# Kernel tuning notes

Measured on AMD Instinct MI355X. Metric: run time of the kernel, lower is better.

## Reference

```python
import jax, jax.numpy as jnp
import numpy as np

H = 128
V = 50000
B = 128
T_C = 50
T_I = 32
T_Q = 32
EPISODES = 3


def gru_cell(x, h, Wih, Whh, bih, bhh):
    # torch GRUCell math
    gi = x @ Wih.T + bih
    gh = h @ Whh.T + bhh
    ir, iz, inn = jnp.split(gi, 3, axis=-1)
    hr, hz, hn = jnp.split(gh, 3, axis=-1)
    r = jax.nn.sigmoid(ir + hr)
    z = jax.nn.sigmoid(iz + hz)
    n = jnp.tanh(inn + r * hn)
    return (1.0 - z) * n + z * h


def gru_outputs(x, Wih, Whh, bih, bhh):
    # x: (N, T, H) -> hidden at every step, (N, T, H)
    h0 = jnp.zeros((x.shape[0], x.shape[2]), x.dtype)
    def step(h, xt):
        h2 = gru_cell(xt, h, Wih, Whh, bih, bhh)
        return h2, h2
    _, ys = jax.lax.scan(step, h0, jnp.swapaxes(x, 0, 1))
    return jnp.swapaxes(ys, 0, 1)


def setup_inputs():
    key = jax.random.key(0)
    ks = iter(jax.random.split(key, 48))
    s = 0.05
    def mat(shape):
        return (jax.random.normal(next(ks), shape) * s).astype(jnp.float32)
    def gru_p(in_dim):
        return mat((3 * H, in_dim)), mat((3 * H, H)), mat((3 * H,)), mat((3 * H,))
    embed = mat((V, H)).at[0].set(0.0)  # padding_idx=0
    ig_Wih, ig_Whh, ig_bih, ig_bhh = gru_p(H)
    qg_Wih, qg_Whh, qg_bih, qg_bhh = gru_p(H)
    at_Wih, at_Whh, at_bih, at_bhh = gru_p(H)
    me_Wih, me_Whh, me_bih, me_bhh = gru_p(H)
    an_Wih, an_Whh, an_bih, an_bhh = gru_p(2 * H)
    gate_W1 = mat((H, 4 * H)); gate_b1 = mat((H,))
    gate_W2 = mat((1, H)); gate_b2 = mat((1,))
    fc_W = mat((V, H)); fc_b = jnp.zeros((V,), jnp.float32)
    facts = jax.random.randint(next(ks), (B, T_C, T_I), 0, V)
    fact_masks = jnp.zeros((B, T_C, T_I), jnp.int32)  # 0 == real token
    questions = jax.random.randint(next(ks), (B, T_Q), 0, V)
    question_masks = jnp.zeros((B, T_Q), jnp.int32)
    return dict(facts=facts, fact_masks=fact_masks, questions=questions,
                question_masks=question_masks, num_decode=8, embed=embed,
                ig_Wih=ig_Wih, ig_Whh=ig_Whh, ig_bih=ig_bih, ig_bhh=ig_bhh,
                qg_Wih=qg_Wih, qg_Whh=qg_Whh, qg_bih=qg_bih, qg_bhh=qg_bhh,
                at_Wih=at_Wih, at_Whh=at_Whh, at_bih=at_bih, at_bhh=at_bhh,
                me_Wih=me_Wih, me_Whh=me_Whh, me_bih=me_bih, me_bhh=me_bhh,
                an_Wih=an_Wih, an_Whh=an_Whh, an_bih=an_bih, an_bhh=an_bhh,
                gate_W1=gate_W1, gate_b1=gate_b1, gate_W2=gate_W2, gate_b2=gate_b2,
                fc_W=fc_W, fc_b=fc_b)


def reference(facts, fact_masks, questions, question_masks, num_decode, embed,
              ig_Wih, ig_Whh, ig_bih, ig_bhh,
              qg_Wih, qg_Whh, qg_bih, qg_bhh,
              at_Wih, at_Whh, at_bih, at_bhh,
              me_Wih, me_Whh, me_bih, me_bhh,
              an_Wih, an_Whh, an_bih, an_bhh,
              gate_W1, gate_b1, gate_W2, gate_b2, fc_W, fc_b):
    Bv, Tc, Ti = facts.shape
    Hd = embed.shape[1]

    # ---- fact encoding: one batched GRU over all B*T_C facts ----
    f = facts.reshape(Bv * Tc, Ti)
    emb = embed[f]                                            # (B*Tc, Ti, H)
    outs = gru_outputs(emb, ig_Wih, ig_Whh, ig_bih, ig_bhh)
    flen = jnp.sum(fact_masks.reshape(Bv * Tc, Ti) == 0, axis=-1)
    enc_f = jnp.take_along_axis(outs, (flen - 1)[:, None, None], axis=1)[:, 0]
    enc_f = enc_f.reshape(Bv, Tc, Hd)                         # (B, T_C, H)

    # ---- question encoding ----
    qouts = gru_outputs(embed[questions], qg_Wih, qg_Whh, qg_bih, qg_bhh)
    qlen = jnp.sum(question_masks == 0, axis=-1)
    q = jnp.take_along_axis(qouts, (qlen - 1)[:, None, None], axis=1)[:, 0]  # (B, H)

    # ---- episodic memory ----
    memory = q
    facts_t = jnp.swapaxes(enc_f, 0, 1)                       # (T_C, B, H)
    for _ in range(EPISODES):
        m = memory
        def ep_step(h, ft):
            z = jnp.concatenate([ft * q, ft * m, jnp.abs(ft - q), jnp.abs(ft - m)], axis=-1)
            g = jax.nn.sigmoid(jnp.tanh(z @ gate_W1.T + gate_b1) @ gate_W2.T + gate_b2)  # (B,1)
            h2 = gru_cell(ft, h, at_Wih, at_Whh, at_bih, at_bhh)
            return g * h2 + (1.0 - g) * h, None
        e, _ = jax.lax.scan(ep_step, jnp.zeros_like(memory), facts_t)
        memory = gru_cell(e, memory, me_Wih, me_Whh, me_bih, me_bhh)

    # ---- answer decoding (y_{t-1} stays the <s> embedding, as in the source) ----
    y0 = jnp.broadcast_to(embed[2], (Bv, Hd))                 # <s> token id = 2
    yq = jnp.concatenate([y0, q], axis=-1)                    # (B, 2H)
    def dec_step(h, _):
        h2 = gru_cell(yq, h, an_Wih, an_Whh, an_bih, an_bhh)
        return h2, jax.nn.log_softmax(h2 @ fc_W.T + fc_b, axis=-1)
    _, dec = jax.lax.scan(dec_step, memory, None, length=num_decode)  # (T, B, V)
    return jnp.swapaxes(dec, 0, 1).reshape(Bv * num_decode, -1)
```

## Files before the change

kernel.cpp:

```cpp
#include <hip/hip_runtime.h>
#include <math.h>

#define H   128
#define H3  384
#define TC  50
#define TI  32
#define TQ  32
#define NB  128
#define NF  (NB*TC)
#define EPISODES 3
#define LSLICE 25

typedef short  bf16x8 __attribute__((ext_vector_type(8)));
typedef float  f32x4  __attribute__((ext_vector_type(4)));

__device__ __forceinline__ float dot4(float4 a, float4 b) {
  return a.x*b.x + a.y*b.y + a.z*b.z + a.w*b.w;
}
__device__ __forceinline__ float sigm(float x) { return 1.f/(1.f + __expf(-x)); }
__device__ __forceinline__ float tanh_f(float x) { return 1.f - 2.f/(1.f + __expf(2.f*x)); }
__device__ __forceinline__ float gru_comb(float ir, float iz, float inn,
                                          float hr, float hz, float hn, float h) {
  float r = sigm(ir + hr);
  float z = sigm(iz + hz);
  float n = tanh_f(inn + r*hn);
  return (1.f - z)*n + z*h;
}
__device__ __forceinline__ short f2bf(float x) {
  union { float f; unsigned u; } v; v.f = x;
  unsigned r = v.u + 0x7fffu + ((v.u >> 16) & 1u);
  return (short)(r >> 16);
}
__device__ __forceinline__ float bf2f(short s) {
  union { unsigned u; float f; } v; v.u = ((unsigned)(unsigned short)s) << 16;
  return v.f;
}
__device__ __forceinline__ bf16x8 pack8(float4 lo, float4 hi) {
  bf16x8 o;
  o[0]=f2bf(lo.x); o[1]=f2bf(lo.y); o[2]=f2bf(lo.z); o[3]=f2bf(lo.w);
  o[4]=f2bf(hi.x); o[5]=f2bf(hi.y); o[6]=f2bf(hi.z); o[7]=f2bf(hi.w);
  return o;
}

__global__ __launch_bounds__(256) void k_mgemm_bf16(const float* __restrict__ A,
    const float* __restrict__ Bm, const float* __restrict__ bias,
    short* __restrict__ C, int M, int N)
{
  __shared__ __align__(16) short As[64][136];
  __shared__ __align__(16) short Bs[128][136];
  int tid = threadIdx.x;
  int lane = tid & 63, wave = tid >> 6;
  int bm = blockIdx.x, bn = blockIdx.y;
  #pragma unroll
  for (int i = 0; i < 4; ++i) {
    int ch = tid + i*256;
    int r = ch >> 4, e = (ch & 15)*8;
    int gr = bm*64 + r; if (gr > M-1) gr = M-1;
    const float* src = A + (size_t)gr*H + e;
    *(bf16x8*)&As[r][e] = pack8(*(const float4*)src, *(const float4*)(src+4));
  }
  #pragma unroll
  for (int i = 0; i < 8; ++i) {
    int ch = tid + i*256;
    int r = ch >> 4, e = (ch & 15)*8;
    int gn = bn*128 + r; if (gn > N-1) gn = N-1;
    const float* src = Bm + (size_t)gn*H + e;
    *(bf16x8*)&Bs[r][e] = pack8(*(const float4*)src, *(const float4*)(src+4));
  }
  __syncthreads();
  int q = lane >> 4, l15 = lane & 15;
  f32x4 acc[8];
  #pragma unroll
  for (int nt = 0; nt < 8; ++nt) { acc[nt][0]=0.f; acc[nt][1]=0.f; acc[nt][2]=0.f; acc[nt][3]=0.f; }
  int mrow = wave*16 + l15;
  #pragma unroll
  for (int kf = 0; kf < 4; ++kf) {
    bf16x8 a = *(bf16x8*)&As[mrow][q*8 + kf*32];
    #pragma unroll
    for (int nt = 0; nt < 8; ++nt) {
      bf16x8 b = *(bf16x8*)&Bs[nt*16 + l15][q*8 + kf*32];
      acc[nt] = __builtin_amdgcn_mfma_f32_16x16x32_bf16(a, b, acc[nt], 0, 0, 0);
    }
  }
  __syncthreads();
  #pragma unroll
  for (int nt = 0; nt < 8; ++nt) {
    int col = nt*16 + l15;
    float bv = bias[bn*128 + col];
    #pragma unroll
    for (int reg = 0; reg < 4; ++reg)
      Bs[wave*16 + q*4 + reg][col] = f2bf(acc[nt][reg] + bv);
  }
  __syncthreads();
  #pragma unroll
  for (int i = 0; i < 4; ++i) {
    int idx = tid + i*256;
    int r = idx >> 4, e = (idx & 15)*8;
    int gr = bm*64 + r;
    if (gr < M) *(bf16x8*)(C + (size_t)gr*N + bn*128 + e) = *(bf16x8*)&Bs[r][e];
  }
}

__global__ __launch_bounds__(128) void k_gather(const float* __restrict__ embed,
    const int* __restrict__ toks, float* __restrict__ dst)
{
  int b = blockIdx.x;
  int t = toks[b];
  dst[(size_t)b*H + threadIdx.x] = embed[(size_t)t*H + threadIdx.x];
}

__global__ __launch_bounds__(256) void k_copy(const float* __restrict__ src,
    float* __restrict__ dst, int n)
{
  int i = blockIdx.x*256 + threadIdx.x;
  if (i < n) dst[i] = src[i];
}

#define GI_STR 392
__global__ __launch_bounds__(512) void k_recgru2(
    const short* __restrict__ GI, const int* __restrict__ toks,
    const int* __restrict__ masks,
    const float* __restrict__ Whh, const float* __restrict__ bhh,
    float* __restrict__ enc_out, int steps)
{
  __shared__ __align__(16) short hsb[2][16][136];
  __shared__ __align__(16) short gib[2][16][GI_STR];
  __shared__ int ltoks[16*TI];
  __shared__ int enc_step_s[16];
  int tid = threadIdx.x;
  int lane = tid & 63, wave = tid >> 6;
  int q = lane >> 4, l15 = lane & 15;
  int seq0 = blockIdx.x * 16;

  for (int i = tid; i < 2*16*136; i += 512) ((short*)hsb)[i] = 0;
  if (toks) for (int i = tid; i < 16*steps; i += 512)
    ltoks[i] = toks[(size_t)seq0*steps + i];
  if (tid < 16) {
    int fl = 0;
    for (int i = 0; i < steps; ++i) fl += (masks[(size_t)(seq0+tid)*steps + i] == 0);
    int et = fl - 1; if (et < 0) et = 0; if (et >= steps) et = steps-1;
    enc_step_s[tid] = et;
  }
  bf16x8 wfrag[3][4];
  #pragma unroll
  for (int i = 0; i < 3; ++i) {
    int n = 16*wave + 128*i + l15;
    const float* wr = Whh + (size_t)n*H + q*8;
    #pragma unroll
    for (int kf = 0; kf < 4; ++kf)
      wfrag[i][kf] = pack8(*(const float4*)(wr + kf*32), *(const float4*)(wr + kf*32 + 4));
  }
  int c = 16*wave + l15;
  float bh0 = bhh[c], bh1 = bhh[c+H], bh2 = bhh[c+2*H];
  int ch0 = tid, ch1 = tid + 512;
  int r0 = ch0/48, o0 = ch0 - r0*48;
  int r1 = ch1/48, o1 = ch1 - r1*48;
  __syncthreads();
  int es[4];
  #pragma unroll
  for (int reg = 0; reg < 4; ++reg) es[reg] = enc_step_s[q*4 + reg];

  {
    size_t row0 = toks ? (size_t)ltoks[r0*steps] : ((size_t)(seq0 + r0)*steps);
    *(bf16x8*)&gib[0][r0][o0*8] = *((const bf16x8*)(GI + row0*H3) + o0);
    if (tid < 256) {
      size_t row1 = toks ? (size_t)ltoks[r1*steps] : ((size_t)(seq0 + r1)*steps);
      *(bf16x8*)&gib[0][r1][o1*8] = *((const bf16x8*)(GI + row1*H3) + o1);
    }
  }
  __syncthreads();

  float hreg[4] = {0.f, 0.f, 0.f, 0.f};
  for (int t = 0; t < steps; ++t) {
    bf16x8 pf0, pf1;
    bool havepf = (t + 1 < steps);
    if (havepf) {
      size_t row0 = toks ? (size_t)ltoks[r0*steps + t + 1]
                         : ((size_t)(seq0 + r0)*steps + t + 1);
      pf0 = *((const bf16x8*)(GI + row0*H3) + o0);
      if (tid < 256) {
        size_t row1 = toks ? (size_t)ltoks[r1*steps + t + 1]
                           : ((size_t)(seq0 + r1)*steps + t + 1);
        pf1 = *((const bf16x8*)(GI + row1*H3) + o1);
      }
    }
    f32x4 acc[3];
    #pragma unroll
    for (int i = 0; i < 3; ++i) { acc[i][0]=0.f; acc[i][1]=0.f; acc[i][2]=0.f; acc[i][3]=0.f; }
    #pragma unroll
    for (int kf = 0; kf < 4; ++kf) {
      bf16x8 a = *(bf16x8*)&hsb[t & 1][l15][kf*32 + q*8];
      #pragma unroll
      for (int i = 0; i < 3; ++i)
        acc[i] = __builtin_amdgcn_mfma_f32_16x16x32_bf16(a, wfrag[i][kf], acc[i], 0, 0, 0);
    }
    #pragma unroll
    for (int reg = 0; reg < 4; ++reg) {
      int row = q*4 + reg;
      float gr = bf2f(gib[t & 1][row][c]);
      float gz = bf2f(gib[t & 1][row][c + 128]);
      float gn = bf2f(gib[t & 1][row][c + 256]);
      float hnew = gru_comb(gr, gz, gn,
                            acc[0][reg] + bh0, acc[1][reg] + bh1, acc[2][reg] + bh2,
                            hreg[reg]);
      hreg[reg] = hnew;
      hsb[(t + 1) & 1][row][c] = f2bf(hnew);
      if (t == es[reg]) enc_out[(size_t)(seq0 + row)*H + c] = hnew;
    }
    if (havepf) {
      *(bf16x8*)&gib[(t + 1) & 1][r0][o0*8] = pf0;
      if (tid < 256) *(bf16x8*)&gib[(t + 1) & 1][r1][o1*8] = pf1;
    }
    __syncthreads();
  }
}

__global__ __launch_bounds__(128) void k_gatepre(const float* __restrict__ encf,
    const float* __restrict__ qv, const float* __restrict__ W1,
    const float* __restrict__ b1, float* __restrict__ U1)
{
  __shared__ float us[16][H], vs[16][H];
  int tid = threadIdx.x;
  int nt0 = blockIdx.x * 16;
  for (int i = tid; i < 16*H; i += 128) {
    int r = i >> 7, k = i & 127;
    int nt = nt0 + r, n = nt / TC;
    float f = encf[(size_t)nt*H + k];
    float q = qv[(size_t)n*H + k];
    us[r][k] = f*q;
    vs[r][k] = fabsf(f - q);
  }
  __syncthreads();
  int c = tid;
  float acc[16] = {};
  const float* wa = W1 + (size_t)c*(4*H);
  const float* wc = wa + 2*H;
  for (int kk = 0; kk < H; kk += 16) {
    float4 a0 = *(const float4*)(wa + kk);
    float4 a1 = *(const float4*)(wa + kk + 4);
    float4 a2 = *(const float4*)(wa + kk + 8);
    float4 a3 = *(const float4*)(wa + kk + 12);
    float4 c0 = *(const float4*)(wc + kk);
    float4 c1 = *(const float4*)(wc + kk + 4);
    float4 c2 = *(const float4*)(wc + kk + 8);
    float4 c3 = *(const float4*)(wc + kk + 12);
    #pragma unroll
    for (int r = 0; r < 16; ++r) {
      const float* up = &us[r][kk];
      const float* vp = &vs[r][kk];
      acc[r] += dot4(*(const float4*)up,     a0) + dot4(*(const float4*)(up+4), a1)
              + dot4(*(const float4*)(up+8), a2) + dot4(*(const float4*)(up+12),a3)
              + dot4(*(const float4*)vp,     c0) + dot4(*(const float4*)(vp+4), c1)
              + dot4(*(const float4*)(vp+8), c2) + dot4(*(const float4*)(vp+12),c3);
    }
  }
  float bb = b1[c];
  #pragma unroll
  for (int r = 0; r < 16; ++r) U1[(size_t)(nt0 + r)*H + c] = acc[r] + bb;
}

__global__ __launch_bounds__(128) void k_gate(const float* __restrict__ encf,
    const float* __restrict__ mem, const float* __restrict__ W1,
    const float* __restrict__ W2, const float* __restrict__ b2,
    const float* __restrict__ U1, float* __restrict__ gate)
{
  __shared__ float us[16][H], vs[16][H], hid[16][H], parts[16][8];
  int tid = threadIdx.x;
  int nt0 = blockIdx.x * 16;
  for (int i = tid; i < 16*H; i += 128) {
    int r = i >> 7, k = i & 127;
    int nt = nt0 + r, n = nt / TC;
    float f = encf[(size_t)nt*H + k];
    float m = mem[(size_t)n*H + k];
    us[r][k] = f*m;
    vs[r][k] = fabsf(f - m);
  }
  __syncthreads();
  int c = tid;
  float acc[16];
  #pragma unroll
  for (int r = 0; r < 16; ++r) acc[r] = U1[(size_t)(nt0 + r)*H + c];
  const float* wb = W1 + (size_t)c*(4*H) + H;
  const float* wd = W1 + (size_t)c*(4*H) + 3*H;
  for (int kk = 0; kk < H; kk += 16) {
    float4 a0 = *(const float4*)(wb + kk);
    float4 a1 = *(const float4*)(wb + kk + 4);
    float4 a2 = *(const float4*)(wb + kk + 8);
    float4 a3 = *(const float4*)(wb + kk + 12);
    float4 c0 = *(const float4*)(wd + kk);
    float4 c1 = *(const float4*)(wd + kk + 4);
    float4 c2 = *(const float4*)(wd + kk + 8);
    float4 c3 = *(const float4*)(wd + kk + 12);
    #pragma unroll
    for (int r = 0; r < 16; ++r) {
      const float* up = &us[r][kk];
      const float* vp = &vs[r][kk];
      acc[r] += dot4(*(const float4*)up,     a0) + dot4(*(const float4*)(up+4), a1)
              + dot4(*(const float4*)(up+8), a2) + dot4(*(const float4*)(up+12),a3)
              + dot4(*(const float4*)vp,     c0) + dot4(*(const float4*)(vp+4), c1)
              + dot4(*(const float4*)(vp+8), c2) + dot4(*(const float4*)(vp+12),c3);
    }
  }
  #pragma unroll
  for (int r = 0; r < 16; ++r) hid[r][c] = tanh_f(acc[r]);
  __syncthreads();
  {
    int r = tid >> 3, i = tid & 7;
    float p = 0.f;
    for (int k = i*16; k < i*16 + 16; ++k) p += hid[r][k]*W2[k];
    parts[r][i] = p;
  }
  __syncthreads();
  if (tid < 16) {
    float s = b2[0];
    #pragma unroll
    for (int i = 0; i < 8; ++i) s += parts[tid][i];
    gate[nt0 + tid] = sigm(s);
  }
}

__global__ __launch_bounds__(512) void k_episode2(
    const short* __restrict__ GIat, const float* __restrict__ gate,
    const float* __restrict__ at_Whh, const float* __restrict__ at_bhh,
    const float* __restrict__ me_Wih, const float* __restrict__ me_Whh,
    const float* __restrict__ me_bih, const float* __restrict__ me_bhh,
    float* __restrict__ mem)
{
  __shared__ __align__(16) short hsb[2][16][136];
  __shared__ __align__(16) short msb[16][136];
  __shared__ __align__(16) short gib[2][16][GI_STR];
  int tid = threadIdx.x;
  int lane = tid & 63, wave = tid >> 6;
  int q = lane >> 4, l15 = lane & 15;
  int n0 = blockIdx.x * 16;

  for (int i = tid; i < 2*16*136; i += 512) ((short*)hsb)[i] = 0;
  for (int i = tid; i < 16*H; i += 512) {
    int r = i >> 7, cc = i & 127;
    msb[r][cc] = f2bf(mem[(size_t)(n0 + r)*H + cc]);
  }
  bf16x8 wfrag[3][4];
  #pragma unroll
  for (int i = 0; i < 3; ++i) {
    int n = 16*wave + 128*i + l15;
    const float* wr = at_Whh + (size_t)n*H + q*8;
    #pragma unroll
    for (int kf = 0; kf < 4; ++kf)
      wfrag[i][kf] = pack8(*(const float4*)(wr + kf*32), *(const float4*)(wr + kf*32 + 4));
  }
  int c = 16*wave + l15;
  float bh0 = at_bhh[c], bh1 = at_bhh[c+H], bh2 = at_bhh[c+2*H];
  int ch0 = tid, ch1 = tid + 512;
  int r0 = ch0/48, o0 = ch0 - r0*48;
  int r1 = ch1/48, o1 = ch1 - r1*48;
  __syncthreads();

  *(bf16x8*)&gib[0][r0][o0*8] = *((const bf16x8*)(GIat + (size_t)(n0 + r0)*TC*H3) + o0);
  if (tid < 256)
    *(bf16x8*)&gib[0][r1][o1*8] = *((const bf16x8*)(GIat + (size_t)(n0 + r1)*TC*H3) + o1);
  __syncthreads();

  float hreg[4] = {0.f, 0.f, 0.f, 0.f};
  for (int t = 0; t < TC; ++t) {
    bf16x8 pf0, pf1;
    bool havepf = (t + 1 < TC);
    if (havepf) {
      pf0 = *((const bf16x8*)(GIat + ((size_t)(n0 + r0)*TC + t + 1)*H3) + o0);
      if (tid < 256)
        pf1 = *((const bf16x8*)(GIat + ((size_t)(n0 + r1)*TC + t + 1)*H3) + o1);
    }
    f32x4 acc[3];
    #pragma unroll
    for (int i = 0; i < 3; ++i) { acc[i][0]=0.f; acc[i][1]=0.f; acc[i][2]=0.f; acc[i][3]=0.f; }
    #pragma unroll
    for (int kf = 0; kf < 4; ++kf) {
      bf16x8 a = *(bf16x8*)&hsb[t & 1][l15][kf*32 + q*8];
      #pragma unroll
      for (int i = 0; i < 3; ++i)
        acc[i] = __builtin_amdgcn_mfma_f32_16x16x32_bf16(a, wfrag[i][kf], acc[i], 0, 0, 0);
    }
    #pragma unroll
    for (int reg = 0; reg < 4; ++reg) {
      int row = q*4 + reg;
      float g  = gate[(size_t)(n0 + row)*TC + t];
      float gr = bf2f(gib[t & 1][row][c]);
      float gz = bf2f(gib[t & 1][row][c + 128]);
      float gn = bf2f(gib[t & 1][row][c + 256]);
      float h2 = gru_comb(gr, gz, gn,
                          acc[0][reg] + bh0, acc[1][reg] + bh1, acc[2][reg] + bh2,
                          hreg[reg]);
      float hnew = g*h2 + (1.f - g)*hreg[reg];
      hreg[reg] = hnew;
      hsb[(t + 1) & 1][row][c] = f2bf(hnew);
    }
    if (havepf) {
      *(bf16x8*)&gib[(t + 1) & 1][r0][o0*8] = pf0;
      if (tid < 256) *(bf16x8*)&gib[(t + 1) & 1][r1][o1*8] = pf1;
    }
    __syncthreads();
  }
  f32x4 gi_acc[3], gh_acc[3];
  #pragma unroll
  for (int i = 0; i < 3; ++i) {
    gi_acc[i][0]=0.f; gi_acc[i][1]=0.f; gi_acc[i][2]=0.f; gi_acc[i][3]=0.f;
    gh_acc[i][0]=0.f; gh_acc[i][1]=0.f; gh_acc[i][2]=0.f; gh_acc[i][3]=0.f;
  }
  #pragma unroll
  for (int i = 0; i < 3; ++i) {
    int n = 16*wave + 128*i + l15;
    const float* wr = me_Wih + (size_t)n*H + q*8;
    #pragma unroll
    for (int kf = 0; kf < 4; ++kf)
      wfrag[i][kf] = pack8(*(const float4*)(wr + kf*32), *(const float4*)(wr + kf*32 + 4));
  }
  #pragma unroll
  for (int kf = 0; kf < 4; ++kf) {
    bf16x8 a = *(bf16x8*)&hsb[TC & 1][l15][kf*32 + q*8];
    #pragma unroll
    for (int i = 0; i < 3; ++i)
      gi_acc[i] = __builtin_amdgcn_mfma_f32_16x16x32_bf16(a, wfrag[i][kf], gi_acc[i], 0, 0, 0);
  }
  #pragma unroll
  for (int i = 0; i < 3; ++i) {
    int n = 16*wave + 128*i + l15;
    const float* wr = me_Whh + (size_t)n*H + q*8;
    #pragma unroll
    for (int kf = 0; kf < 4; ++kf)
      wfrag[i][kf] = pack8(*(const float4*)(wr + kf*32), *(const float4*)(wr + kf*32 + 4));
  }
  #pragma unroll
  for (int kf = 0; kf < 4; ++kf) {
    bf16x8 a = *(bf16x8*)&msb[l15][kf*32 + q*8];
    #pragma unroll
    for (int i = 0; i < 3; ++i)
      gh_acc[i] = __builtin_amdgcn_mfma_f32_16x16x32_bf16(a, wfrag[i][kf], gh_acc[i], 0, 0, 0);
  }
  float bi0 = me_bih[c], bi1 = me_bih[c+H], bi2 = me_bih[c+2*H];
  float bo0 = me_bhh[c], bo1 = me_bhh[c+H], bo2 = me_bhh[c+2*H];
  #pragma unroll
  for (int reg = 0; reg < 4; ++reg) {
    int row = q*4 + reg;
    float m = mem[(size_t)(n0 + row)*H + c];
    float mnew = gru_comb(gi_acc[0][reg] + bi0, gi_acc[1][reg] + bi1, gi_acc[2][reg] + bi2,
                          gh_acc[0][reg] + bo0, gh_acc[1][reg] + bo1, gh_acc[2][reg] + bo2, m);
    mem[(size_t)(n0 + row)*H + c] = mnew;
  }
}

__global__ __launch_bounds__(384) void k_decode(const float* __restrict__ embed,
    const float* __restrict__ qv, const float* __restrict__ mem,
    const float* __restrict__ an_Wih, const float* __restrict__ an_Whh,
    const float* __restrict__ an_bih, const float* __restrict__ an_bhh,
    float* __restrict__ h2d, int ND)
{
  __shared__ float hs[2][H], qs[2][H], e2[H], ghs[2][H3], gis[2][H3];
  int tid = threadIdx.x;
  int n0 = blockIdx.x * 2;
  if (tid < H) e2[tid] = embed[2*H + tid];
  if (tid < 256) {
    int r = tid >> 7, c = tid & 127;
    hs[r][c] = mem[(size_t)(n0 + r)*H + c];
    qs[r][c] = qv[(size_t)(n0 + r)*H + c];
  }
  __syncthreads();
  {
    const float* wp = an_Wih + (size_t)tid*(2*H);
    float se = 0.f, sq0 = 0.f, sq1 = 0.f;
    for (int kk = 0; kk < H; kk += 16) {
      float4 w0 = *(const float4*)(wp + kk);
      float4 w1 = *(const float4*)(wp + kk + 4);
      float4 w2 = *(const float4*)(wp + kk + 8);
      float4 w3 = *(const float4*)(wp + kk + 12);
      const float* ep = &e2[kk];
      se += dot4(*(const float4*)ep,     w0) + dot4(*(const float4*)(ep+4), w1)
          + dot4(*(const float4*)(ep+8), w2) + dot4(*(const float4*)(ep+12),w3);
      float4 u0 = *(const float4*)(wp + H + kk);
      float4 u1 = *(const float4*)(wp + H + kk + 4);
      float4 u2 = *(const float4*)(wp + H + kk + 8);
      float4 u3 = *(const float4*)(wp + H + kk + 12);
      const float* q0 = &qs[0][kk];
      const float* q1 = &qs[1][kk];
      sq0 += dot4(*(const float4*)q0,     u0) + dot4(*(const float4*)(q0+4), u1)
           + dot4(*(const float4*)(q0+8), u2) + dot4(*(const float4*)(q0+12),u3);
      sq1 += dot4(*(const float4*)q1,     u0) + dot4(*(const float4*)(q1+4), u1)
           + dot4(*(const float4*)(q1+8), u2) + dot4(*(const float4*)(q1+12),u3);
    }
    float b = an_bih[tid];
    gis[0][tid] = b + se + sq0;
    gis[1][tid] = b + se + sq1;
  }
  const float* whp = an_Whh + (size_t)tid*H;
  float bh = an_bhh[tid];
  for (int t = 0; t < ND; ++t) {
    float a0 = 0.f, a1 = 0.f;
    for (int kk = 0; kk < H; kk += 16) {
      float4 w0 = *(const float4*)(whp + kk);
      float4 w1 = *(const float4*)(whp + kk + 4);
      float4 w2 = *(const float4*)(whp + kk + 8);
      float4 w3 = *(const float4*)(whp + kk + 12);
      const float* h0p = &hs[0][kk];
      const float* h1p = &hs[1][kk];
      a0 += dot4(*(const float4*)h0p,     w0) + dot4(*(const float4*)(h0p+4), w1)
          + dot4(*(const float4*)(h0p+8), w2) + dot4(*(const float4*)(h0p+12),w3);
      a1 += dot4(*(const float4*)h1p,     w0) + dot4(*(const float4*)(h1p+4), w1)
          + dot4(*(const float4*)(h1p+8), w2) + dot4(*(const float4*)(h1p+12),w3);
    }
    ghs[0][tid] = a0 + bh;
    ghs[1][tid] = a1 + bh;
    __syncthreads();
    if (tid < 256) {
      int r = tid >> 7, c = tid & 127;
      float h2 = gru_comb(gis[r][c], gis[r][c+H], gis[r][c+2*H],
                          ghs[r][c], ghs[r][c+H], ghs[r][c+2*H], hs[r][c]);
      hs[r][c] = h2;
      h2d[((size_t)(n0 + r)*ND + t)*H + c] = h2;
    }
    __syncthreads();
  }
}

__global__ __launch_bounds__(256) void k_lpass1(const float* __restrict__ A,
    const float* __restrict__ Bm, const float* __restrict__ bias,
    float2* __restrict__ partials, int M, int N)
{
  __shared__ __align__(16) short As[64][136];
  __shared__ __align__(16) short Bs[128][136];
  int tid = threadIdx.x;
  int lane = tid & 63, wave = tid >> 6;
  int q = lane >> 4, l15 = lane & 15;
  int bm = blockIdx.x, sl = blockIdx.y;
  #pragma unroll
  for (int i = 0; i < 4; ++i) {
    int ch = tid + i*256;
    int r = ch >> 4, e = (ch & 15)*8;
    int gr = bm*64 + r; if (gr > M-1) gr = M-1;
    const float* src = A + (size_t)gr*H + e;
    *(bf16x8*)&As[r][e] = pack8(*(const float4*)src, *(const float4*)(src+4));
  }
  int mrow = wave*16 + l15;
  float m[4] = {-3.4e38f, -3.4e38f, -3.4e38f, -3.4e38f};
  float s[4] = {0.f, 0.f, 0.f, 0.f};
  for (int chn = 0; chn < 16; ++chn) {
    int c0 = sl*2048 + chn*128;
    #pragma unroll
    for (int i = 0; i < 8; ++i) {
      int ch = tid + i*256;
      int r = ch >> 4, e = (ch & 15)*8;
      int gn = c0 + r; if (gn > N-1) gn = N-1;
      const float* src = Bm + (size_t)gn*H + e;
      *(bf16x8*)&Bs[r][e] = pack8(*(const float4*)src, *(const float4*)(src+4));
    }
    __syncthreads();
    f32x4 acc[8];
    #pragma unroll
    for (int nt = 0; nt < 8; ++nt) { acc[nt][0]=0.f; acc[nt][1]=0.f; acc[nt][2]=0.f; acc[nt][3]=0.f; }
    #pragma unroll
    for (int kf = 0; kf < 4; ++kf) {
      bf16x8 a = *(bf16x8*)&As[mrow][q*8 + kf*32];
      #pragma unroll
      for (int nt = 0; nt < 8; ++nt) {
        bf16x8 b = *(bf16x8*)&Bs[nt*16 + l15][q*8 + kf*32];
        acc[nt] = __builtin_amdgcn_mfma_f32_16x16x32_bf16(a, b, acc[nt], 0, 0, 0);
      }
    }
    __syncthreads();
    float bv[8];
    #pragma unroll
    for (int nt = 0; nt < 8; ++nt) {
      int col = c0 + nt*16 + l15;
      bv[nt] = (col < N) ? bias[col] : 0.f;
    }
    #pragma unroll
    for (int reg = 0; reg < 4; ++reg) {
      float xs[8], cm = -3.4e38f;
      #pragma unroll
      for (int nt = 0; nt < 8; ++nt) {
        int col = c0 + nt*16 + l15;
        float x = (col < N) ? (acc[nt][reg] + bv[nt]) : -3.4e38f;
        xs[nt] = x; cm = fmaxf(cm, x);
      }
      float nm = fmaxf(m[reg], cm);
      float ss = s[reg] * __expf(m[reg] - nm);
      #pragma unroll
      for (int nt = 0; nt < 8; ++nt) ss += __expf(xs[nt] - nm);
      m[reg] = nm; s[reg] = ss;
    }
  }
  #pragma unroll
  for (int off = 1; off < 16; off <<= 1) {
    #pragma unroll
    for (int reg = 0; reg < 4; ++reg) {
      float mo = __shfl_xor(m[reg], off);
      float so = __shfl_xor(s[reg], off);
      float nm = fmaxf(m[reg], mo);
      s[reg] = s[reg]*__expf(m[reg] - nm) + so*__expf(mo - nm);
      m[reg] = nm;
    }
  }
  if (l15 == 0) {
    #pragma unroll
    for (int reg = 0; reg < 4; ++reg) {
      int row = bm*64 + wave*16 + q*4 + reg;
      if (row < M) partials[(size_t)row*LSLICE + sl] = make_float2(m[reg], s[reg]);
    }
  }
}

__global__ __launch_bounds__(256) void k_lse(const float2* __restrict__ partials,
                                             float* __restrict__ lse, int M)
{
  int row = blockIdx.x*256 + threadIdx.x;
  if (row >= M) return;
  float m = -3.4e38f, s = 0.f;
  for (int i = 0; i < LSLICE; ++i) {
    float2 p = partials[(size_t)row*LSLICE + i];
    float nm = fmaxf(m, p.x);
    s = s*__expf(m - nm) + p.y*__expf(p.x - nm);
    m = nm;
  }
  lse[row] = m + logf(s);
}

__global__ __launch_bounds__(256) void k_lpass2(const float* __restrict__ A,
    const float* __restrict__ Bm, const float* __restrict__ bias,
    const float* __restrict__ lse, float* __restrict__ C, int M, int N)
{
  __shared__ __align__(16) short As[64][136];
  __shared__ __align__(16) short Bs[128][136];
  int tid = threadIdx.x;
  int lane = tid & 63, wave = tid >> 6;
  int q = lane >> 4, l15 = lane & 15;
  int bm = blockIdx.x, bn = blockIdx.y;
  #pragma unroll
  for (int i = 0; i < 4; ++i) {
    int ch = tid + i*256;
    int r = ch >> 4, e = (ch & 15)*8;
    int gr = bm*64 + r; if (gr > M-1) gr = M-1;
    const float* src = A + (size_t)gr*H + e;
    *(bf16x8*)&As[r][e] = pack8(*(const float4*)src, *(const float4*)(src+4));
  }
  #pragma unroll
  for (int i = 0; i < 8; ++i) {
    int ch = tid + i*256;
    int r = ch >> 4, e = (ch & 15)*8;
    int gn = bn*128 + r; if (gn > N-1) gn = N-1;
    const float* src = Bm + (size_t)gn*H + e;
    *(bf16x8*)&Bs[r][e] = pack8(*(const float4*)src, *(const float4*)(src+4));
  }
  __syncthreads();
  f32x4 acc[8];
  #pragma unroll
  for (int nt = 0; nt < 8; ++nt) { acc[nt][0]=0.f; acc[nt][1]=0.f; acc[nt][2]=0.f; acc[nt][3]=0.f; }
  int mrow = wave*16 + l15;
  #pragma unroll
  for (int kf = 0; kf < 4; ++kf) {
    bf16x8 a = *(bf16x8*)&As[mrow][q*8 + kf*32];
    #pragma unroll
    for (int nt = 0; nt < 8; ++nt) {
      bf16x8 b = *(bf16x8*)&Bs[nt*16 + l15][q*8 + kf*32];
      acc[nt] = __builtin_amdgcn_mfma_f32_16x16x32_bf16(a, b, acc[nt], 0, 0, 0);
    }
  }
  __syncthreads();
  float (*Cs)[132] = (float(*)[132])&Bs[0][0];
  float lrow[4];
  #pragma unroll
  for (int reg = 0; reg < 4; ++reg) {
    int row = bm*64 + wave*16 + q*4 + reg;
    lrow[reg] = lse[row < M ? row : M-1];
  }
  #pragma unroll
  for (int nt = 0; nt < 8; ++nt) {
    int col = nt*16 + l15;
    int gcol = bn*128 + col;
    float bv = (gcol < N) ? bias[gcol] : 0.f;
    #pragma unroll
    for (int reg = 0; reg < 4; ++reg)
      Cs[wave*16 + q*4 + reg][col] = acc[nt][reg] + bv - lrow[reg];
  }
  __syncthreads();
  #pragma unroll
  for (int i = 0; i < 8; ++i) {
    int idx = tid + i*256;
    int r = idx >> 5, c4 = (idx & 31)*4;
    int gr = bm*64 + r;
    int gc = bn*128 + c4;
    if (gr < M && gc + 3 < N)
      *(float4*)(C + (size_t)gr*N + gc) = *(float4*)&Cs[r][c4];
    else if (gr < M) {
      #pragma unroll
      for (int j = 0; j < 4; ++j)
        if (gc + j < N) C[(size_t)gr*N + gc + j] = Cs[r][c4 + j];
    }
  }
}

extern "C" void kernel_launch(void* const* d_in, const int* in_sizes, int n_in,
                              void* d_out, int out_size, void* d_ws, size_t ws_size,
                              hipStream_t stream) {
  const int*   facts     = (const int*)  d_in[0];
  const int*   fmask     = (const int*)  d_in[1];
  const int*   questions = (const int*)  d_in[2];
  const int*   qmask     = (const int*)  d_in[3];
  const float* embed     = (const float*)d_in[5];
  const float* ig_Wih    = (const float*)d_in[6];
  const float* ig_Whh    = (const float*)d_in[7];
  const float* ig_bih    = (const float*)d_in[8];
  const float* ig_bhh    = (const float*)d_in[9];
  const float* qg_Wih    = (const float*)d_in[10];
  const float* qg_Whh    = (const float*)d_in[11];
  const float* qg_bih    = (const float*)d_in[12];
  const float* qg_bhh    = (const float*)d_in[13];
  const float* at_Wih    = (const float*)d_in[14];
  const float* at_Whh    = (const float*)d_in[15];
  const float* at_bih    = (const float*)d_in[16];
  const float* at_bhh    = (const float*)d_in[17];
  const float* me_Wih    = (const float*)d_in[18];
  const float* me_Whh    = (const float*)d_in[19];
  const float* me_bih    = (const float*)d_in[20];
  const float* me_bhh    = (const float*)d_in[21];
  const float* an_Wih    = (const float*)d_in[22];
  const float* an_Whh    = (const float*)d_in[23];
  const float* an_bih    = (const float*)d_in[24];
  const float* an_bhh    = (const float*)d_in[25];
  const float* gate_W1   = (const float*)d_in[26];
  const float* gate_b1   = (const float*)d_in[27];
  const float* gate_W2   = (const float*)d_in[28];
  const float* gate_b2   = (const float*)d_in[29];
  const float* fc_W      = (const float*)d_in[30];
  const float* fc_b      = (const float*)d_in[31];
  (void)n_in; (void)ws_size;

  const int V  = in_sizes[5] / H;
  const int ND = out_size / (NB * V);
  const int M  = NB * ND;

  float* OUT = (float*)d_out;
  size_t oP    = 0;
  size_t oEMBQ = (size_t)V * 192;
  size_t oQGI  = oEMBQ + (size_t)NB*TQ*H;
  size_t oGIAT = oQGI  + (size_t)NB*TQ*192;
  size_t oU1   = oGIAT + (size_t)NF*192;
  size_t oGATE = oU1   + (size_t)NF*H;
  short* Psh    = (short*)(OUT + oP);
  float* EMBQ   = OUT + oEMBQ;
  short* QGIsh  = (short*)(OUT + oQGI);
  short* GIATsh = (short*)(OUT + oGIAT);
  float* U1b    = OUT + oU1;
  float* GATE   = OUT + oGATE;

  float* encf = (float*)d_ws;
  float* qvec = encf + (size_t)NF*H;
  float* mem  = qvec + (size_t)NB*H;
  float* h2d  = mem  + (size_t)NB*H;
  float* lse  = h2d  + (size_t)M*H;
  float2* partials = (float2*)(lse + M);

  k_mgemm_bf16<<<dim3((V+63)/64, H3/128), 256, 0, stream>>>(embed, ig_Wih, ig_bih, Psh, V, H3);
  k_gather<<<NB*TQ, 128, 0, stream>>>(embed, questions, EMBQ);
  k_mgemm_bf16<<<dim3(NB*TQ/64, H3/128), 256, 0, stream>>>(EMBQ, qg_Wih, qg_bih, QGIsh, NB*TQ, H3);
  k_recgru2<<<NF/16, 512, 0, stream>>>(Psh, facts, fmask, ig_Whh, ig_bhh, encf, TI);
  k_recgru2<<<NB/16, 512, 0, stream>>>(QGIsh, nullptr, qmask, qg_Whh, qg_bhh, qvec, TQ);
  k_mgemm_bf16<<<dim3(NF/64, H3/128), 256, 0, stream>>>(encf, at_Wih, at_bih, GIATsh, NF, H3);
  k_gatepre<<<NF/16, 128, 0, stream>>>(encf, qvec, gate_W1, gate_b1, U1b);
  k_copy<<<(NB*H+255)/256, 256, 0, stream>>>(qvec, mem, NB*H);
  for (int e = 0; e < EPISODES; ++e) {
    k_gate<<<NF/16, 128, 0, stream>>>(encf, mem, gate_W1, gate_W2, gate_b2, U1b, GATE);
    k_episode2<<<NB/16, 512, 0, stream>>>(GIATsh, GATE, at_Whh, at_bhh,
                                          me_Wih, me_Whh, me_bih, me_bhh, mem);
  }
  k_decode<<<NB/2, 384, 0, stream>>>(embed, qvec, mem, an_Wih, an_Whh, an_bih, an_bhh,
                                     h2d, ND);
  k_lpass1<<<dim3(M/64, LSLICE), 256, 0, stream>>>(h2d, fc_W, fc_b, partials, M, V);
  k_lse<<<(M+255)/256, 256, 0, stream>>>(partials, lse, M);
  k_lpass2<<<dim3(M/64, (V+127)/128), 256, 0, stream>>>(h2d, fc_W, fc_b, lse, OUT, M, V);
}
```

Measured before the change: 1.000 ms.

## Pre-convert embed, fc_W and input weights to bf16 once; widen fact GRU tiles

A single conversion kernel now writes bf16 copies of the embedding table, fc_W and the three input-projection weight matrices. The GEMMs and both logit passes then load bf16 directly instead of converting fp32 per tile, which cuts repeated conversion work and global read volume, especially for the vocabulary-sized fc_W that every row block re-reads. The fc_W bf16 copy is staged in the output buffer's last row block, so that block is computed last from the fp32 source. The fact GRU now processes 25 sequences per block (two MFMA row tiles) instead of 16, and the decoder writes bf16 hidden states.

```diff
diff --git a/kernel.cpp b/kernel.cpp
--- a/kernel.cpp
+++ b/kernel.cpp
@@ -12,6 +12,7 @@
 #define LSLICE 25
 
 typedef short  bf16x8 __attribute__((ext_vector_type(8)));
+typedef short  bf16x4 __attribute__((ext_vector_type(4)));
 typedef float  f32x4  __attribute__((ext_vector_type(4)));
 
 __device__ __forceinline__ float dot4(float4 a, float4 b) {
@@ -42,30 +43,72 @@
   return o;
 }
 
-__global__ __launch_bounds__(256) void k_mgemm_bf16(const float* __restrict__ A,
-    const float* __restrict__ Bm, const float* __restrict__ bias,
-    short* __restrict__ C, int M, int N)
+__global__ __launch_bounds__(256) void k_cvtall(
+    const float* __restrict__ emb, short* __restrict__ emb16,
+    const float* __restrict__ fcw, short* __restrict__ fcw16,
+    const float* __restrict__ w0, const float* __restrict__ w1,
+    const float* __restrict__ w2, short* __restrict__ w16, int VH)
+{
+  int bid = blockIdx.x;
+  const float* src; short* dst; int n, b0, nb;
+  if (bid < 1280)      { src = emb; dst = emb16; n = VH; b0 = 0;    nb = 1280; }
+  else if (bid < 2560) { src = fcw; dst = fcw16; n = VH; b0 = 1280; nb = 1280; }
+  else {
+    int j = (bid - 2560) / 24;
+    src = (j == 0) ? w0 : ((j == 1) ? w1 : w2);
+    dst = w16 + (size_t)j*H3*H;
+    n = H3*H; b0 = 2560 + j*24; nb = 24;
+  }
+  int stride = nb*256*8;
+  for (int i = ((bid - b0)*256 + threadIdx.x)*8; i < n; i += stride) {
+    float4 lo = *(const float4*)(src + i);
+    float4 hi = *(const float4*)(src + i + 4);
+    *(bf16x8*)(dst + i) = pack8(lo, hi);
+  }
+}
+
+__global__ __launch_bounds__(256) void k_gather16(const short* __restrict__ emb16,
+    const int* __restrict__ toks, short* __restrict__ dst)
+{
+  int b0 = blockIdx.x * 8;
+  int r = threadIdx.x >> 5, cc = (threadIdx.x & 31)*4;
+  int t = toks[b0 + r];
+  *(bf16x4*)(dst + (size_t)(b0 + r)*H + cc) = *(const bf16x4*)(emb16 + (size_t)t*H + cc);
+}
+
+__global__ __launch_bounds__(256) void k_mgemmX(const short* __restrict__ A16,
+    const float* __restrict__ A32, const short* __restrict__ B16,
+    const float* __restrict__ bias, short* __restrict__ C, int M, int N)
 {
   __shared__ __align__(16) short As[64][136];
   __shared__ __align__(16) short Bs[128][136];
   int tid = threadIdx.x;
   int lane = tid & 63, wave = tid >> 6;
   int bm = blockIdx.x, bn = blockIdx.y;
-  #pragma unroll
-  for (int i = 0; i < 4; ++i) {
-    int ch = tid + i*256;
-    int r = ch >> 4, e = (ch & 15)*8;
-    int gr = bm*64 + r; if (gr > M-1) gr = M-1;
-    const float* src = A + (size_t)gr*H + e;
-    *(bf16x8*)&As[r][e] = pack8(*(const float4*)src, *(const float4*)(src+4));
+  if (A16) {
+    #pragma unroll
+    for (int i = 0; i < 4; ++i) {
+      int ch = tid + i*256;
+      int r = ch >> 4, e = (ch & 15)*8;
+      int gr = bm*64 + r; if (gr > M-1) gr = M-1;
+      *(bf16x8*)&As[r][e] = *(const bf16x8*)(A16 + (size_t)gr*H + e);
+    }
+  } else {
+    #pragma unroll
+    for (int i = 0; i < 4; ++i) {
+      int ch = tid + i*256;
+      int r = ch >> 4, e = (ch & 15)*8;
+      int gr = bm*64 + r; if (gr > M-1) gr = M-1;
+      const float* src = A32 + (size_t)gr*H + e;
+      *(bf16x8*)&As[r][e] = pack8(*(const float4*)src, *(const float4*)(src+4));
+    }
   }
   #pragma unroll
   for (int i = 0; i < 8; ++i) {
     int ch = tid + i*256;
     int r = ch >> 4, e = (ch & 15)*8;
     int gn = bn*128 + r; if (gn > N-1) gn = N-1;
-    const float* src = Bm + (size_t)gn*H + e;
-    *(bf16x8*)&Bs[r][e] = pack8(*(const float4*)src, *(const float4*)(src+4));
+    *(bf16x8*)&Bs[r][e] = *(const bf16x8*)(B16 + (size_t)gn*H + e);
   }
   __syncthreads();
   int q = lane >> 4, l15 = lane & 15;
@@ -99,14 +142,6 @@
     int gr = bm*64 + r;
     if (gr < M) *(bf16x8*)(C + (size_t)gr*N + bn*128 + e) = *(bf16x8*)&Bs[r][e];
   }
-}
-
-__global__ __launch_bounds__(128) void k_gather(const float* __restrict__ embed,
-    const int* __restrict__ toks, float* __restrict__ dst)
-{
-  int b = blockIdx.x;
-  int t = toks[b];
-  dst[(size_t)b*H + threadIdx.x] = embed[(size_t)t*H + threadIdx.x];
 }
 
 __global__ __launch_bounds__(256) void k_copy(const float* __restrict__ src,
@@ -215,6 +250,116 @@
   }
 }
 
+__global__ __launch_bounds__(512) void k_recgru3(
+    const short* __restrict__ GI, const int* __restrict__ toks,
+    const int* __restrict__ masks,
+    const float* __restrict__ Whh, const float* __restrict__ bhh,
+    float* __restrict__ enc_out, int steps)
+{
+  __shared__ __align__(16) short hsb[2][32][136];
+  __shared__ __align__(16) short gib[2][25][GI_STR];
+  __shared__ int ltoks[25*TI];
+  __shared__ int enc_step_s[25];
+  int tid = threadIdx.x;
+  int lane = tid & 63, wave = tid >> 6;
+  int q = lane >> 4, l15 = lane & 15;
+  int seq0 = blockIdx.x * 25;
+
+  for (int i = tid; i < 2*32*136; i += 512) ((short*)hsb)[i] = 0;
+  for (int i = tid; i < 25*steps; i += 512)
+    ltoks[i] = toks[(size_t)seq0*steps + i];
+  if (tid < 25) {
+    int fl = 0;
+    for (int i = 0; i < steps; ++i) fl += (masks[(size_t)(seq0+tid)*steps + i] == 0);
+    int et = fl - 1; if (et < 0) et = 0; if (et >= steps) et = steps-1;
+    enc_step_s[tid] = et;
+  }
+  bf16x8 wfrag[3][4];
+  #pragma unroll
+  for (int i = 0; i < 3; ++i) {
+    int n = 16*wave + 128*i + l15;
+    const float* wr = Whh + (size_t)n*H + q*8;
+    #pragma unroll
+    for (int kf = 0; kf < 4; ++kf)
+      wfrag[i][kf] = pack8(*(const float4*)(wr + kf*32), *(const float4*)(wr + kf*32 + 4));
+  }
+  int c = 16*wave + l15;
+  float bh0 = bhh[c], bh1 = bhh[c+H], bh2 = bhh[c+2*H];
+  int ch0 = tid, ch1 = tid + 512, ch2 = tid + 1024;
+  int r0 = ch0/48, o0 = ch0 - r0*48;
+  int r1 = ch1/48, o1 = ch1 - r1*48;
+  int r2 = ch2/48, o2 = ch2 - r2*48;
+  __syncthreads();
+  int es0[4], es1[4];
+  #pragma unroll
+  for (int reg = 0; reg < 4; ++reg) {
+    es0[reg] = enc_step_s[q*4 + reg];
+    int row2 = 16 + q*4 + reg;
+    es1[reg] = (row2 < 25) ? enc_step_s[row2] : -9;
+  }
+  {
+    *(bf16x8*)&gib[0][r0][o0*8] = *((const bf16x8*)(GI + (size_t)ltoks[r0*steps]*H3) + o0);
+    *(bf16x8*)&gib[0][r1][o1*8] = *((const bf16x8*)(GI + (size_t)ltoks[r1*steps]*H3) + o1);
+    if (tid < 176)
+      *(bf16x8*)&gib[0][r2][o2*8] = *((const bf16x8*)(GI + (size_t)ltoks[r2*steps]*H3) + o2);
+  }
+  __syncthreads();
+
+  float h0[4] = {0.f,0.f,0.f,0.f}, h1[4] = {0.f,0.f,0.f,0.f};
+  for (int t = 0; t < steps; ++t) {
+    bf16x8 pf0, pf1, pf2;
+    bool havepf = (t + 1 < steps);
+    if (havepf) {
+      pf0 = *((const bf16x8*)(GI + (size_t)ltoks[r0*steps + t + 1]*H3) + o0);
+      pf1 = *((const bf16x8*)(GI + (size_t)ltoks[r1*steps + t + 1]*H3) + o1);
+      if (tid < 176)
+        pf2 = *((const bf16x8*)(GI + (size_t)ltoks[r2*steps + t + 1]*H3) + o2);
+    }
+    f32x4 acc0[3], acc1[3];
+    acc0[0] = (f32x4){bh0,bh0,bh0,bh0};
+    acc0[1] = (f32x4){bh1,bh1,bh1,bh1};
+    acc0[2] = (f32x4){bh2,bh2,bh2,bh2};
+    acc1[0] = acc0[0]; acc1[1] = acc0[1]; acc1[2] = acc0[2];
+    #pragma unroll
+    for (int kf = 0; kf < 4; ++kf) {
+      bf16x8 a0 = *(bf16x8*)&hsb[t & 1][l15][kf*32 + q*8];
+      bf16x8 a1 = *(bf16x8*)&hsb[t & 1][16 + l15][kf*32 + q*8];
+      #pragma unroll
+      for (int i = 0; i < 3; ++i) {
+        acc0[i] = __builtin_amdgcn_mfma_f32_16x16x32_bf16(a0, wfrag[i][kf], acc0[i], 0, 0, 0);
+        acc1[i] = __builtin_amdgcn_mfma_f32_16x16x32_bf16(a1, wfrag[i][kf], acc1[i], 0, 0, 0);
+      }
+    }
+    #pragma unroll
+    for (int reg = 0; reg < 4; ++reg) {
+      int row = q*4 + reg;
+      float gr = bf2f(gib[t & 1][row][c]);
+      float gz = bf2f(gib[t & 1][row][c + 128]);
+      float gn = bf2f(gib[t & 1][row][c + 256]);
+      float hnew = gru_comb(gr, gz, gn, acc0[0][reg], acc0[1][reg], acc0[2][reg], h0[reg]);
+      h0[reg] = hnew;
+      hsb[(t + 1) & 1][row][c] = f2bf(hnew);
+      if (t == es0[reg]) enc_out[(size_t)(seq0 + row)*H + c] = hnew;
+      int row2 = row + 16;
+      if (row2 < 25) {
+        float gr2 = bf2f(gib[t & 1][row2][c]);
+        float gz2 = bf2f(gib[t & 1][row2][c + 128]);
+        float gn2 = bf2f(gib[t & 1][row2][c + 256]);
+        float hnew2 = gru_comb(gr2, gz2, gn2, acc1[0][reg], acc1[1][reg], acc1[2][reg], h1[reg]);
+        h1[reg] = hnew2;
+        hsb[(t + 1) & 1][row2][c] = f2bf(hnew2);
+        if (t == es1[reg]) enc_out[(size_t)(seq0 + row2)*H + c] = hnew2;
+      }
+    }
+    if (havepf) {
+      *(bf16x8*)&gib[(t + 1) & 1][r0][o0*8] = pf0;
+      *(bf16x8*)&gib[(t + 1) & 1][r1][o1*8] = pf1;
+      if (tid < 176) *(bf16x8*)&gib[(t + 1) & 1][r2][o2*8] = pf2;
+    }
+    __syncthreads();
+  }
+}
+
 __global__ __launch_bounds__(128) void k_gatepre(const float* __restrict__ encf,
     const float* __restrict__ qv, const float* __restrict__ W1,
     const float* __restrict__ b1, float* __restrict__ U1)
@@ -451,7 +596,7 @@
     const float* __restrict__ qv, const float* __restrict__ mem,
     const float* __restrict__ an_Wih, const float* __restrict__ an_Whh,
     const float* __restrict__ an_bih, const float* __restrict__ an_bhh,
-    float* __restrict__ h2d, int ND)
+    short* __restrict__ h2d16, int ND)
 {
   __shared__ float hs[2][H], qs[2][H], e2[H], ghs[2][H3], gis[2][H3];
   int tid = threadIdx.x;
@@ -513,14 +658,14 @@
       float h2 = gru_comb(gis[r][c], gis[r][c+H], gis[r][c+2*H],
                           ghs[r][c], ghs[r][c+H], ghs[r][c+2*H], hs[r][c]);
       hs[r][c] = h2;
-      h2d[((size_t)(n0 + r)*ND + t)*H + c] = h2;
+      h2d16[((size_t)(n0 + r)*ND + t)*H + c] = f2bf(h2);
     }
     __syncthreads();
   }
 }
 
-__global__ __launch_bounds__(256) void k_lpass1(const float* __restrict__ A,
-    const float* __restrict__ Bm, const float* __restrict__ bias,
+__global__ __launch_bounds__(256) void k_lpass1(const short* __restrict__ A16,
+    const short* __restrict__ B16, const float* __restrict__ bias,
     float2* __restrict__ partials, int M, int N)
 {
   __shared__ __align__(16) short As[64][136];
@@ -534,8 +679,7 @@
     int ch = tid + i*256;
     int r = ch >> 4, e = (ch & 15)*8;
     int gr = bm*64 + r; if (gr > M-1) gr = M-1;
-    const float* src = A + (size_t)gr*H + e;
-    *(bf16x8*)&As[r][e] = pack8(*(const float4*)src, *(const float4*)(src+4));
+    *(bf16x8*)&As[r][e] = *(const bf16x8*)(A16 + (size_t)gr*H + e);
   }
   int mrow = wave*16 + l15;
   float m[4] = {-3.4e38f, -3.4e38f, -3.4e38f, -3.4e38f};
@@ -547,8 +691,7 @@
       int ch = tid + i*256;
       int r = ch >> 4, e = (ch & 15)*8;
       int gn = c0 + r; if (gn > N-1) gn = N-1;
-      const float* src = Bm + (size_t)gn*H + e;
-      *(bf16x8*)&Bs[r][e] = pack8(*(const float4*)src, *(const float4*)(src+4));
+      *(bf16x8*)&Bs[r][e] = *(const bf16x8*)(B16 + (size_t)gn*H + e);
     }
     __syncthreads();
     f32x4 acc[8];
@@ -621,31 +764,41 @@
   lse[row] = m + logf(s);
 }
 
-__global__ __launch_bounds__(256) void k_lpass2(const float* __restrict__ A,
-    const float* __restrict__ Bm, const float* __restrict__ bias,
-    const float* __restrict__ lse, float* __restrict__ C, int M, int N)
+__global__ __launch_bounds__(256) void k_lpass2(const short* __restrict__ A16,
+    const short* __restrict__ B16, const float* __restrict__ B32,
+    const float* __restrict__ bias, const float* __restrict__ lse,
+    float* __restrict__ C, int M, int N, int bm_off)
 {
   __shared__ __align__(16) short As[64][136];
   __shared__ __align__(16) short Bs[128][136];
   int tid = threadIdx.x;
   int lane = tid & 63, wave = tid >> 6;
   int q = lane >> 4, l15 = lane & 15;
-  int bm = blockIdx.x, bn = blockIdx.y;
+  int bm = blockIdx.x + bm_off, bn = blockIdx.y;
   #pragma unroll
   for (int i = 0; i < 4; ++i) {
     int ch = tid + i*256;
     int r = ch >> 4, e = (ch & 15)*8;
     int gr = bm*64 + r; if (gr > M-1) gr = M-1;
-    const float* src = A + (size_t)gr*H + e;
-    *(bf16x8*)&As[r][e] = pack8(*(const float4*)src, *(const float4*)(src+4));
-  }
-  #pragma unroll
-  for (int i = 0; i < 8; ++i) {
-    int ch = tid + i*256;
-    int r = ch >> 4, e = (ch & 15)*8;
-    int gn = bn*128 + r; if (gn > N-1) gn = N-1;
-    const float* src = Bm + (size_t)gn*H + e;
-    *(bf16x8*)&Bs[r][e] = pack8(*(const float4*)src, *(const float4*)(src+4));
+    *(bf16x8*)&As[r][e] = *(const bf16x8*)(A16 + (size_t)gr*H + e);
+  }
+  if (B16) {
+    #pragma unroll
+    for (int i = 0; i < 8; ++i) {
+      int ch = tid + i*256;
+      int r = ch >> 4, e = (ch & 15)*8;
+      int gn = bn*128 + r; if (gn > N-1) gn = N-1;
+      *(bf16x8*)&Bs[r][e] = *(const bf16x8*)(B16 + (size_t)gn*H + e);
+    }
+  } else {
+    #pragma unroll
+    for (int i = 0; i < 8; ++i) {
+      int ch = tid + i*256;
+      int r = ch >> 4, e = (ch & 15)*8;
+      int gn = bn*128 + r; if (gn > N-1) gn = N-1;
+      const float* src = B32 + (size_t)gn*H + e;
+      *(bf16x8*)&Bs[r][e] = pack8(*(const float4*)src, *(const float4*)(src+4));
+    }
   }
   __syncthreads();
   f32x4 acc[8];
@@ -734,34 +887,44 @@
   const int V  = in_sizes[5] / H;
   const int ND = out_size / (NB * V);
   const int M  = NB * ND;
+  const int BMT = M / 64;
 
   float* OUT = (float*)d_out;
-  size_t oP    = 0;
-  size_t oEMBQ = (size_t)V * 192;
-  size_t oQGI  = oEMBQ + (size_t)NB*TQ*H;
-  size_t oGIAT = oQGI  + (size_t)NB*TQ*192;
-  size_t oU1   = oGIAT + (size_t)NF*192;
-  size_t oGATE = oU1   + (size_t)NF*H;
+  size_t oP     = 0;
+  size_t oEMB16 = (size_t)V*192;
+  size_t oEMBQ  = oEMB16 + (size_t)V*64;
+  size_t oQGI   = oEMBQ + (size_t)NB*TQ*64;
+  size_t oGIAT  = oQGI  + (size_t)NB*TQ*192;
+  size_t oU1    = oGIAT + (size_t)NF*192;
+  size_t oGATE  = oU1   + (size_t)NF*H;
+  size_t oW16   = oGATE + NF;
   short* Psh    = (short*)(OUT + oP);
-  float* EMBQ   = OUT + oEMBQ;
+  short* EMB16  = (short*)(OUT + oEMB16);
+  short* EMBQ16 = (short*)(OUT + oEMBQ);
   short* QGIsh  = (short*)(OUT + oQGI);
   short* GIATsh = (short*)(OUT + oGIAT);
   float* U1b    = OUT + oU1;
   float* GATE   = OUT + oGATE;
-
-  float* encf = (float*)d_ws;
-  float* qvec = encf + (size_t)NF*H;
-  float* mem  = qvec + (size_t)NB*H;
-  float* h2d  = mem  + (size_t)NB*H;
-  float* lse  = h2d  + (size_t)M*H;
+  short* igW16  = (short*)(OUT + oW16);
+  short* qgW16  = igW16 + (size_t)H3*H;
+  short* atW16  = qgW16 + (size_t)H3*H;
+  short* FCW16  = (short*)(OUT + (size_t)(M - 64)*V);
+
+  float* encf  = (float*)d_ws;
+  float* qvec  = encf + (size_t)NF*H;
+  float* mem   = qvec + (size_t)NB*H;
+  short* H2D16 = (short*)(mem + (size_t)NB*H);
+  float* lse   = (float*)(H2D16 + (size_t)M*H);
   float2* partials = (float2*)(lse + M);
 
-  k_mgemm_bf16<<<dim3((V+63)/64, H3/128), 256, 0, stream>>>(embed, ig_Wih, ig_bih, Psh, V, H3);
-  k_gather<<<NB*TQ, 128, 0, stream>>>(embed, questions, EMBQ);
-  k_mgemm_bf16<<<dim3(NB*TQ/64, H3/128), 256, 0, stream>>>(EMBQ, qg_Wih, qg_bih, QGIsh, NB*TQ, H3);
-  k_recgru2<<<NF/16, 512, 0, stream>>>(Psh, facts, fmask, ig_Whh, ig_bhh, encf, TI);
+  k_cvtall<<<2632, 256, 0, stream>>>(embed, EMB16, fc_W, FCW16,
+                                     ig_Wih, qg_Wih, at_Wih, igW16, V*H);
+  k_mgemmX<<<dim3((V+63)/64, H3/128), 256, 0, stream>>>(EMB16, nullptr, igW16, ig_bih, Psh, V, H3);
+  k_gather16<<<NB*TQ/8, 256, 0, stream>>>(EMB16, questions, EMBQ16);
+  k_mgemmX<<<dim3(NB*TQ/64, H3/128), 256, 0, stream>>>(EMBQ16, nullptr, qgW16, qg_bih, QGIsh, NB*TQ, H3);
+  k_recgru3<<<NF/25, 512, 0, stream>>>(Psh, facts, fmask, ig_Whh, ig_bhh, encf, TI);
   k_recgru2<<<NB/16, 512, 0, stream>>>(QGIsh, nullptr, qmask, qg_Whh, qg_bhh, qvec, TQ);
-  k_mgemm_bf16<<<dim3(NF/64, H3/128), 256, 0, stream>>>(encf, at_Wih, at_bih, GIATsh, NF, H3);
+  k_mgemmX<<<dim3(NF/64, H3/128), 256, 0, stream>>>(nullptr, encf, atW16, at_bih, GIATsh, NF, H3);
   k_gatepre<<<NF/16, 128, 0, stream>>>(encf, qvec, gate_W1, gate_b1, U1b);
   k_copy<<<(NB*H+255)/256, 256, 0, stream>>>(qvec, mem, NB*H);
   for (int e = 0; e < EPISODES; ++e) {
@@ -770,8 +933,11 @@
                                           me_Wih, me_Whh, me_bih, me_bhh, mem);
   }
   k_decode<<<NB/2, 384, 0, stream>>>(embed, qvec, mem, an_Wih, an_Whh, an_bih, an_bhh,
-                                     h2d, ND);
-  k_lpass1<<<dim3(M/64, LSLICE), 256, 0, stream>>>(h2d, fc_W, fc_b, partials, M, V);
+                                     H2D16, ND);
+  k_lpass1<<<dim3(BMT, LSLICE), 256, 0, stream>>>(H2D16, FCW16, fc_b, partials, M, V);
   k_lse<<<(M+255)/256, 256, 0, stream>>>(partials, lse, M);
-  k_lpass2<<<dim3(M/64, (V+127)/128), 256, 0, stream>>>(h2d, fc_W, fc_b, lse, OUT, M, V);
-}
+  k_lpass2<<<dim3(BMT-1, (V+127)/128), 256, 0, stream>>>(H2D16, FCW16, nullptr, fc_b, lse,
+                                                         OUT, M, V, 0);
+  k_lpass2<<<dim3(1, (V+127)/128), 256, 0, stream>>>(H2D16, nullptr, fc_W, fc_b, lse,
+                                                     OUT, M, V, BMT-1);
+}
```

New measurement: 978.7 us. -2.2%, faster.
